# Performance work log

Measured on AMD Instinct MI355X. Metric: run time of the kernel, lower is better.

The kernel has to match this reference:

```python
import jax, jax.numpy as jnp
import numpy as np

N_BATCHES = 32
N_LABELS = 100


def setup_inputs() -> dict:
    key = jax.random.key(0)
    ks = jax.random.split(key, 7)
    N, D, P = 16384, 2048, 256
    x = jax.random.normal(ks[0], (N, D), dtype=jnp.float32)
    label = jax.random.randint(ks[1], (N,), 0, N_LABELS, dtype=jnp.int64)
    label_batch = jnp.sort(jax.random.randint(ks[2], (N,), 0, N_BATCHES, dtype=jnp.int64))
    W1_w = jax.random.normal(ks[3], (P, D), dtype=jnp.float32) * 0.02
    W1_b = jax.random.normal(ks[4], (P,), dtype=jnp.float32) * 0.02
    W2_w = jax.random.normal(ks[5], (P, D), dtype=jnp.float32) * 0.02
    W2_b = jax.random.normal(ks[6], (P,), dtype=jnp.float32) * 0.02
    return {"x": x, "label": label, "label_batch": label_batch,
            "W1_w": W1_w, "W1_b": W1_b, "W2_w": W2_w, "W2_b": W2_b}


def _loo_diff_label_mean(x, label, label_batch):
    # For each sample i: mean of x over {j : label_batch[j]==label_batch[i] and label[j]!=label[i]}.
    # Rows with no such j are zero (torch code's `continue`). x is detached in the original.
    N = x.shape[0]
    xs = jax.lax.stop_gradient(x)
    seg = label_batch * N_LABELS + label                      # combined (group,label) key
    n_seg = N_BATCHES * N_LABELS
    ones = jnp.ones((N,), dtype=x.dtype)
    sum_bl = jax.ops.segment_sum(xs, seg, num_segments=n_seg)            # [n_seg, D]
    cnt_bl = jax.ops.segment_sum(ones, seg, num_segments=n_seg)          # [n_seg]
    sum_b = jax.ops.segment_sum(xs, label_batch, num_segments=N_BATCHES)  # [NB, D]
    cnt_b = jax.ops.segment_sum(ones, label_batch, num_segments=N_BATCHES)
    diff_sum = sum_b[label_batch] - sum_bl[seg]               # [N, D]
    diff_cnt = cnt_b[label_batch] - cnt_bl[seg]               # [N]
    safe = jnp.maximum(diff_cnt, 1.0)
    mean = diff_sum / safe[:, None]
    return jnp.where((diff_cnt > 0)[:, None], mean, jnp.zeros_like(mean))


def reference(x, label, label_batch, W1_w, W1_b, W2_w, W2_b):
    calc_mean = _loo_diff_label_mean(x, label, label_batch)   # detached aggregate
    return x @ W1_w.T + W1_b + calc_mean @ W2_w.T + W2_b      # W1(x) + W2(mean)
```

## Files before the change

kernel.cpp:

```cpp
#include <hip/hip_runtime.h>
#include <cstdint>

#define N_SAMPLES 16384
#define DIM 2048
#define PDIM 256
#define NB 32
#define NL 100
#define NSEG (NB * NL)

typedef float floatx4 __attribute__((ext_vector_type(4)));
typedef __bf16 bf16x8 __attribute__((ext_vector_type(8)));

__device__ __forceinline__ unsigned short f32_to_bf16(float f) {
    unsigned int u = __float_as_uint(f);
    u += 0x7fffu + ((u >> 16) & 1u);
    return (unsigned short)(u >> 16);
}

__global__ __launch_bounds__(256) void prep_kernel(
    const float* __restrict__ W1w, const float* __restrict__ W1b,
    const float* __restrict__ W2w, const float* __restrict__ W2b,
    const int* __restrict__ label, const int* __restrict__ lbatch,
    unsigned short* __restrict__ Wbf, float* __restrict__ bias,
    int* __restrict__ seg, int* __restrict__ cnt, float* __restrict__ SW2)
{
    int i = blockIdx.x * 256 + threadIdx.x;
    Wbf[i]              = f32_to_bf16(W1w[i]);
    Wbf[PDIM * DIM + i] = f32_to_bf16(W2w[i]);
    if (i < PDIM) bias[i] = W1b[i] + W2b[i];
    if (i < N_SAMPLES) seg[i] = lbatch[i] * NL + label[i];
    if (i < NSEG) cnt[i] = 0;
    if (i < NSEG * PDIM / 2) ((float2*)SW2)[i] = make_float2(0.f, 0.f);
}

__global__ __launch_bounds__(256) void hist_kernel(
    const int* __restrict__ seg, int* __restrict__ cnt)
{
    int i = blockIdx.x * 256 + threadIdx.x;
    atomicAdd(&cnt[seg[i]], 1);
}

__global__ __launch_bounds__(256) void gemm512_kernel(
    const float* __restrict__ x,
    const unsigned short* __restrict__ Wbf,
    const float* __restrict__ bias, const int* __restrict__ seg,
    float* __restrict__ out, float* __restrict__ SW2)
{
    constexpr int BM = 128, BN = 128, BK = 32;
    __shared__ __align__(16) float ldsAf[BM * BK];
    __shared__ __align__(16) unsigned short ldsB[BN * BK];
    const int tid = threadIdx.x;
    const int lane = tid & 63;
    const int wave = tid >> 6;
    const int wr = wave >> 1, wc = wave & 1;
    const int quad = lane >> 4, l15 = lane & 15;
    const int m0 = blockIdx.x * BM;
    const int n0 = blockIdx.y * BN;

    const int arow = lane >> 3;
    const int achk = (lane & 7) ^ arow;
    const int brow = lane >> 2, bchk = lane & 3;

    floatx4 acc[4][4];
    #pragma unroll
    for (int i = 0; i < 4; ++i)
        #pragma unroll
        for (int j = 0; j < 4; ++j) acc[i][j] = (floatx4){0.f, 0.f, 0.f, 0.f};

    const float* Asrc = x + (size_t)(m0 + arow) * DIM + achk * 4;
    const unsigned short* Bsrc = Wbf + (size_t)(n0 + brow) * DIM + bchk * 8;

    for (int kk = 0; kk < DIM; kk += BK) {
        __syncthreads();
        #pragma unroll
        for (int ch = wave; ch < 16; ch += 4)
            __builtin_amdgcn_global_load_lds(
                (const __attribute__((address_space(1))) void*)(Asrc + (size_t)ch * 8 * DIM + kk),
                (__attribute__((address_space(3))) void*)&ldsAf[ch * 256], 16, 0, 0);
        #pragma unroll
        for (int ch = wave; ch < 8; ch += 4)
            __builtin_amdgcn_global_load_lds(
                (const __attribute__((address_space(1))) void*)(Bsrc + (size_t)ch * 16 * DIM + kk),
                (__attribute__((address_space(3))) void*)&ldsB[ch * 512], 16, 0, 0);
        __syncthreads();

        bf16x8 af[4], bf[4];
        #pragma unroll
        for (int mi = 0; mi < 4; ++mi) {
            const int ar = wr * 64 + mi * 16 + l15;
            const int s = ar & 7;
            const float* pa = &ldsAf[ar * BK];
            floatx4 lo = *(const floatx4*)(pa + (((quad * 2)     ^ s) << 2));
            floatx4 hi = *(const floatx4*)(pa + (((quad * 2 + 1) ^ s) << 2));
            af[mi] = (bf16x8){ (__bf16)lo[0], (__bf16)lo[1], (__bf16)lo[2], (__bf16)lo[3],
                               (__bf16)hi[0], (__bf16)hi[1], (__bf16)hi[2], (__bf16)hi[3] };
        }
        #pragma unroll
        for (int ni = 0; ni < 4; ++ni)
            bf[ni] = *(const bf16x8*)&ldsB[(wc * 64 + ni * 16 + l15) * BK + quad * 8];
        #pragma unroll
        for (int mi = 0; mi < 4; ++mi)
            #pragma unroll
            for (int ni = 0; ni < 4; ++ni)
                acc[mi][ni] = __builtin_amdgcn_mfma_f32_16x16x32_bf16(
                    af[mi], bf[ni], acc[mi][ni], 0, 0, 0);
    }

    if (n0 < PDIM) {
        #pragma unroll
        for (int mi = 0; mi < 4; ++mi) {
            const int rbase = m0 + wr * 64 + mi * 16 + quad * 4;
            #pragma unroll
            for (int ni = 0; ni < 4; ++ni) {
                const int col = n0 + wc * 64 + ni * 16 + l15;
                const float bs = bias[col];
                #pragma unroll
                for (int r = 0; r < 4; ++r)
                    out[(size_t)(rbase + r) * PDIM + col] = acc[mi][ni][r] + bs;
            }
        }
    } else {
        const int c0 = n0 - PDIM;
        #pragma unroll
        for (int mi = 0; mi < 4; ++mi) {
            const int rbase = m0 + wr * 64 + mi * 16 + quad * 4;
            #pragma unroll
            for (int r = 0; r < 4; ++r) {
                const int sr = seg[rbase + r];
                #pragma unroll
                for (int ni = 0; ni < 4; ++ni) {
                    const int col = c0 + wc * 64 + ni * 16 + l15;
                    atomicAdd(&SW2[(size_t)sr * PDIM + col], acc[mi][ni][r]);
                }
            }
        }
    }
}

__global__ __launch_bounds__(256) void finalize_kernel(
    float* __restrict__ SW2, const int* __restrict__ cnt)
{
    const int b = blockIdx.x;
    const int col = threadIdx.x;
    int cb = 0;
    #pragma unroll 4
    for (int l = 0; l < NL; ++l) cb += cnt[b * NL + l];
    float tot = 0.f;
    #pragma unroll 4
    for (int l = 0; l < NL; ++l)
        tot += SW2[(size_t)(b * NL + l) * PDIM + col];
    for (int l = 0; l < NL; ++l) {
        const int s = b * NL + l;
        const int dc = cb - cnt[s];
        const float v = SW2[(size_t)s * PDIM + col];
        SW2[(size_t)s * PDIM + col] = (dc > 0) ? (tot - v) / (float)dc : 0.f;
    }
}

__global__ __launch_bounds__(256) void epilogue_kernel(
    float* __restrict__ out, const float* __restrict__ SW2,
    const int* __restrict__ seg)
{
    const int idx = blockIdx.x * 256 + threadIdx.x;
    const int row = idx >> 6;
    const int c = (idx & 63) * 4;
    float4 v = ((const float4*)out)[idx];
    const float4 s4 = *(const float4*)&SW2[(size_t)seg[row] * PDIM + c];
    v.x += s4.x; v.y += s4.y; v.z += s4.z; v.w += s4.w;
    ((float4*)out)[idx] = v;
}

extern "C" void kernel_launch(void* const* d_in, const int* in_sizes, int n_in,
                              void* d_out, int out_size, void* d_ws, size_t ws_size,
                              hipStream_t stream)
{
    const float* x      = (const float*)d_in[0];
    const int*   label  = (const int*)d_in[1];
    const int*   lbatch = (const int*)d_in[2];
    const float* W1w    = (const float*)d_in[3];
    const float* W1b    = (const float*)d_in[4];
    const float* W2w    = (const float*)d_in[5];
    const float* W2b    = (const float*)d_in[6];
    float* out = (float*)d_out;

    char* ws = (char*)d_ws;
    size_t off = 0;
    auto alloc = [&](size_t bytes) {
        void* p = ws + off;
        off = (off + bytes + 255) & ~(size_t)255;
        return p;
    };
    unsigned short* Wbf = (unsigned short*)alloc((size_t)2 * PDIM * DIM * 2);
    float* SW2  = (float*)alloc((size_t)NSEG * PDIM * 4);
    float* bias = (float*)alloc(PDIM * 4);
    int*   seg  = (int*)alloc(N_SAMPLES * 4);
    int*   cnt  = (int*)alloc(NSEG * 4);

    prep_kernel<<<PDIM * DIM / 256, 256, 0, stream>>>(
        W1w, W1b, W2w, W2b, label, lbatch, Wbf, bias, seg, cnt, SW2);

    hist_kernel<<<N_SAMPLES / 256, 256, 0, stream>>>(seg, cnt);

    gemm512_kernel<<<dim3(N_SAMPLES / 128, 4), 256, 0, stream>>>(
        x, Wbf, bias, seg, out, SW2);

    finalize_kernel<<<NB, 256, 0, stream>>>(SW2, cnt);

    epilogue_kernel<<<(size_t)N_SAMPLES * PDIM / 4 / 256, 256, 0, stream>>>(
        out, SW2, seg);
}
```

Baseline: 286.9 us.

## Retile GEMM to 64x128x64 with per-wave column split and swizzled B

Shrinks the GEMM block tile from 128x128 to 64 rows while doubling the K step to 64. Each wave now owns all 64 rows and 32 columns, and the B tile in LDS gets an XOR swizzle. Launch bounds request 4 blocks per CU. The aim is twice as many blocks for better occupancy and fewer barriers per K, at the cost of re-reading the full W tile for every 64-row block and doing more A fp32-to-bf16 conversion per MFMA.

```diff
diff --git a/kernel.cpp b/kernel.cpp
--- a/kernel.cpp
+++ b/kernel.cpp
@@ -40,79 +40,87 @@
     atomicAdd(&cnt[seg[i]], 1);
 }
 
-__global__ __launch_bounds__(256) void gemm512_kernel(
+__global__ __launch_bounds__(256, 4) void gemm512_kernel(
     const float* __restrict__ x,
     const unsigned short* __restrict__ Wbf,
     const float* __restrict__ bias, const int* __restrict__ seg,
     float* __restrict__ out, float* __restrict__ SW2)
 {
-    constexpr int BM = 128, BN = 128, BK = 32;
+    constexpr int BM = 64, BN = 128, BK = 64;
     __shared__ __align__(16) float ldsAf[BM * BK];
     __shared__ __align__(16) unsigned short ldsB[BN * BK];
     const int tid = threadIdx.x;
     const int lane = tid & 63;
     const int wave = tid >> 6;
-    const int wr = wave >> 1, wc = wave & 1;
     const int quad = lane >> 4, l15 = lane & 15;
     const int m0 = blockIdx.x * BM;
     const int n0 = blockIdx.y * BN;
 
-    const int arow = lane >> 3;
-    const int achk = (lane & 7) ^ arow;
-    const int brow = lane >> 2, bchk = lane & 3;
-
-    floatx4 acc[4][4];
+    const int arow = lane >> 4;
+    const int achk = (lane & 15) ^ ((wave & 1) * 4 + arow);
+    const int brow = lane >> 3;
+    const int bchk = (lane & 7) ^ brow;
+
+    floatx4 acc[4][2];
     #pragma unroll
     for (int i = 0; i < 4; ++i)
         #pragma unroll
-        for (int j = 0; j < 4; ++j) acc[i][j] = (floatx4){0.f, 0.f, 0.f, 0.f};
+        for (int j = 0; j < 2; ++j) acc[i][j] = (floatx4){0.f, 0.f, 0.f, 0.f};
 
     const float* Asrc = x + (size_t)(m0 + arow) * DIM + achk * 4;
     const unsigned short* Bsrc = Wbf + (size_t)(n0 + brow) * DIM + bchk * 8;
 
+    const int swa = l15 & 7;
+
     for (int kk = 0; kk < DIM; kk += BK) {
         __syncthreads();
         #pragma unroll
         for (int ch = wave; ch < 16; ch += 4)
             __builtin_amdgcn_global_load_lds(
-                (const __attribute__((address_space(1))) void*)(Asrc + (size_t)ch * 8 * DIM + kk),
+                (const __attribute__((address_space(1))) void*)(Asrc + (size_t)ch * 4 * DIM + kk),
                 (__attribute__((address_space(3))) void*)&ldsAf[ch * 256], 16, 0, 0);
         #pragma unroll
-        for (int ch = wave; ch < 8; ch += 4)
+        for (int ch = wave; ch < 16; ch += 4)
             __builtin_amdgcn_global_load_lds(
-                (const __attribute__((address_space(1))) void*)(Bsrc + (size_t)ch * 16 * DIM + kk),
+                (const __attribute__((address_space(1))) void*)(Bsrc + (size_t)ch * 8 * DIM + kk),
                 (__attribute__((address_space(3))) void*)&ldsB[ch * 512], 16, 0, 0);
         __syncthreads();
 
-        bf16x8 af[4], bf[4];
+        #pragma unroll
+        for (int ks = 0; ks < 2; ++ks) {
+            bf16x8 af[4], bf[2];
+            #pragma unroll
+            for (int mi = 0; mi < 4; ++mi) {
+                const int ar = mi * 16 + l15;
+                const int q0 = ks * 8 + quad * 2;
+                const float* pa = &ldsAf[ar * BK];
+                floatx4 lo = *(const floatx4*)(pa + (((q0)     ^ swa) << 2));
+                floatx4 hi = *(const floatx4*)(pa + (((q0 + 1) ^ swa) << 2));
+                af[mi] = (bf16x8){ (__bf16)lo[0], (__bf16)lo[1], (__bf16)lo[2], (__bf16)lo[3],
+                                   (__bf16)hi[0], (__bf16)hi[1], (__bf16)hi[2], (__bf16)hi[3] };
+            }
+            #pragma unroll
+            for (int ni = 0; ni < 2; ++ni) {
+                const int br = wave * 32 + ni * 16 + l15;
+                const int q = ks * 4 + quad;
+                bf[ni] = *(const bf16x8*)&ldsB[br * BK + (((q) ^ swa) << 3)];
+            }
+            #pragma unroll
+            for (int mi = 0; mi < 4; ++mi)
+                #pragma unroll
+                for (int ni = 0; ni < 2; ++ni)
+                    acc[mi][ni] = __builtin_amdgcn_mfma_f32_16x16x32_bf16(
+                        af[mi], bf[ni], acc[mi][ni], 0, 0, 0);
+        }
+    }
+
+    if (n0 < PDIM) {
         #pragma unroll
         for (int mi = 0; mi < 4; ++mi) {
-            const int ar = wr * 64 + mi * 16 + l15;
-            const int s = ar & 7;
-            const float* pa = &ldsAf[ar * BK];
-            floatx4 lo = *(const floatx4*)(pa + (((quad * 2)     ^ s) << 2));
-            floatx4 hi = *(const floatx4*)(pa + (((quad * 2 + 1) ^ s) << 2));
-            af[mi] = (bf16x8){ (__bf16)lo[0], (__bf16)lo[1], (__bf16)lo[2], (__bf16)lo[3],
-                               (__bf16)hi[0], (__bf16)hi[1], (__bf16)hi[2], (__bf16)hi[3] };
-        }
-        #pragma unroll
-        for (int ni = 0; ni < 4; ++ni)
-            bf[ni] = *(const bf16x8*)&ldsB[(wc * 64 + ni * 16 + l15) * BK + quad * 8];
-        #pragma unroll
-        for (int mi = 0; mi < 4; ++mi)
-            #pragma unroll
-            for (int ni = 0; ni < 4; ++ni)
-                acc[mi][ni] = __builtin_amdgcn_mfma_f32_16x16x32_bf16(
-                    af[mi], bf[ni], acc[mi][ni], 0, 0, 0);
-    }
-
-    if (n0 < PDIM) {
-        #pragma unroll
-        for (int mi = 0; mi < 4; ++mi) {
-            const int rbase = m0 + wr * 64 + mi * 16 + quad * 4;
-            #pragma unroll
-            for (int ni = 0; ni < 4; ++ni) {
-                const int col = n0 + wc * 64 + ni * 16 + l15;
+            const int rbase = m0 + mi * 16 + quad * 4;
+            #pragma unroll
+            for (int ni = 0; ni < 2; ++ni) {
+                const int col = n0 + wave * 32 + ni * 16 + l15;
                 const float bs = bias[col];
                 #pragma unroll
                 for (int r = 0; r < 4; ++r)
@@ -123,13 +131,13 @@
         const int c0 = n0 - PDIM;
         #pragma unroll
         for (int mi = 0; mi < 4; ++mi) {
-            const int rbase = m0 + wr * 64 + mi * 16 + quad * 4;
+            const int rbase = m0 + mi * 16 + quad * 4;
             #pragma unroll
             for (int r = 0; r < 4; ++r) {
                 const int sr = seg[rbase + r];
                 #pragma unroll
-                for (int ni = 0; ni < 4; ++ni) {
-                    const int col = c0 + wc * 64 + ni * 16 + l15;
+                for (int ni = 0; ni < 2; ++ni) {
+                    const int col = c0 + wave * 32 + ni * 16 + l15;
                     atomicAdd(&SW2[(size_t)sr * PDIM + col], acc[mi][ni][r]);
                 }
             }
@@ -201,7 +209,7 @@
 
     hist_kernel<<<N_SAMPLES / 256, 256, 0, stream>>>(seg, cnt);
 
-    gemm512_kernel<<<dim3(N_SAMPLES / 128, 4), 256, 0, stream>>>(
+    gemm512_kernel<<<dim3(N_SAMPLES / 64, 4), 256, 0, stream>>>(
         x, Wbf, bias, seg, out, SW2);
 
     finalize_kernel<<<NB, 256, 0, stream>>>(SW2, cnt);
```

New measurement: 271.5 us. 1.06x faster.
